# Optimization experiments

Hardware: AMD Instinct MI355X
Metric: run time of the kernel (lower is better)

The kernel has to match this reference:

```python
import jax, jax.numpy as jnp
import numpy as np

CPG = 2          # channels_per_group
WH, WW = 227, 227  # window_size
EPS = 1e-05


def setup_inputs() -> dict:
    key = jax.random.key(0)
    x = jax.random.normal(key, (8, 32, 512, 512), dtype=jnp.float32)
    weight = jnp.ones((1, 32, 1, 1), dtype=jnp.float32)
    bias = jnp.zeros((1, 32, 1, 1), dtype=jnp.float32)
    return {"x": x, "weight": weight, "bias": bias}


def _box_sum(ii, wh, ww):
    # ii: integral image (N,C,H,W); returns window sums of size (wh,ww)
    # over rows h+1..h+wh, cols w+1..w+ww -> (N,C,H-wh,W-ww)
    return (ii[:, :, wh:, ww:] - ii[:, :, :-wh, ww:]
            - ii[:, :, wh:, :-ww] + ii[:, :, :-wh, :-ww])


def reference(x, weight, bias):
    N, C, H, W = x.shape
    G = C // CPG
    # window_size (227,227) < (H,W)=(512,512): integral-image branch
    ii = jnp.cumsum(jnp.cumsum(x, axis=2), axis=3)
    ii_sq = jnp.cumsum(jnp.cumsum(x * x, axis=2), axis=3)
    h, w = H - WH, W - WW
    # per-channel box sums, then sum over channels_per_group -> (N,G,h,w)
    sums = _box_sum(ii, WH, WW).reshape(N, G, CPG, h, w).sum(axis=2)
    squares = _box_sum(ii_sq, WH, WW).reshape(N, G, CPG, h, w).sum(axis=2)
    n = WH * WW * CPG
    means = sums / n
    var = (squares - sums * sums / n) / n
    # replicate-pad stats back to (H,W): (left,right,top,bottom) like F.pad
    pt, pb = (H - h) // 2, H - h - (H - h) // 2
    pl, pr = (W - w) // 2, W - w - (W - w) // 2
    pad = ((0, 0), (0, 0), (pt, pb), (pl, pr))
    p_means = jnp.pad(means, pad, mode='edge')
    p_vars = jnp.pad(var, pad, mode='edge') + EPS
    # torch computes sums/squares under no_grad -> stats are constants
    p_means = jax.lax.stop_gradient(p_means)
    p_vars = jax.lax.stop_gradient(p_vars)
    xg = x.reshape(N, G, CPG, H, W)
    out = (xg - p_means[:, :, None]) / jnp.sqrt(p_vars)[:, :, None]
    out = out.reshape(N, C, H, W)
    return out * weight + bias
```

## Files before the change

### kernel.cpp

```cpp
#include <hip/hip_runtime.h>

namespace {
constexpr int Hn = 512, Wn = 512;
constexpr int WHn = 227, WWn = 227;
constexpr int OHn = Hn - WHn;
constexpr int OWn = Wn - WWn;
constexpr int PTn = 113, PLn = 113;
constexpr float EPSn = 1e-5f;
}

__global__ __launch_bounds__(512, 4) void lcn_fused(const float* __restrict__ x,
                                                    const float* __restrict__ weight,
                                                    const float* __restrict__ bias,
                                                    float* __restrict__ out) {
  const int B = blockIdx.x;
  const int X = B & 7;
  const int s = B >> 3;
  const int chunk = s & 3;
  const int g = X * 16 + (s >> 2);
  const int w = threadIdx.x;
  const int lane = w & 63;
  const int wid = w >> 6;

  const float* __restrict__ x0 = x + (size_t)(g * 2) * Hn * Wn;
  const float* __restrict__ x1 = x0 + (size_t)Hn * Wn;
  float* __restrict__ o0 = out + (size_t)(g * 2) * Hn * Wn;
  float* __restrict__ o1 = o0 + (size_t)Hn * Wn;
  const int cch = (g & 15) * 2;
  const float wt0 = weight[cch], wt1 = weight[cch + 1];
  const float bs0 = bias[cch], bs1 = bias[cch + 1];

  const int h0 = chunk == 0 ? 0 : chunk == 1 ? 48 : chunk == 2 ? 144 : 240;
  const int h1 = chunk == 0 ? 48 : chunk == 1 ? 144 : chunk == 2 ? 240 : 285;

  __shared__ __align__(16) float2 Ps[2][8][Wn + 1];
  __shared__ float2 wsum[8][8];
  __shared__ float2 bstat[4][132];

  const int q = w & 127;
  const int p = w >> 7;
  float4 sS = {0.f, 0.f, 0.f, 0.f}, sQ = {0.f, 0.f, 0.f, 0.f};
  {
    const float4* __restrict__ r0 =
        reinterpret_cast<const float4*>(x0 + (size_t)(h0 + 1) * Wn) + q;
    const float4* __restrict__ r1 =
        reinterpret_cast<const float4*>(x1 + (size_t)(h0 + 1) * Wn) + q;
    #pragma unroll 8
    for (int r = p; r < WHn; r += 4) {
      float4 a = r0[(size_t)r * (Wn / 4)];
      float4 b = r1[(size_t)r * (Wn / 4)];
      sS.x += a.x + b.x; sQ.x += a.x * a.x + b.x * b.x;
      sS.y += a.y + b.y; sQ.y += a.y * a.y + b.y * b.y;
      sS.z += a.z + b.z; sQ.z += a.z * a.z + b.z * b.z;
      sS.w += a.w + b.w; sQ.w += a.w * a.w + b.w * b.w;
    }
  }
  float accS, accQ;
  {
    float4* cc = reinterpret_cast<float4*>(&Ps[0][0][0]);
    cc[p * 256 + 2 * q]     = make_float4(sS.x, sQ.x, sS.y, sQ.y);
    cc[p * 256 + 2 * q + 1] = make_float4(sS.z, sQ.z, sS.w, sQ.w);
    __syncthreads();
    const float2* cf = reinterpret_cast<const float2*>(&Ps[0][0][0]);
    float2 t0 = cf[0 * Wn + w], t1 = cf[1 * Wn + w];
    float2 t2 = cf[2 * Wn + w], t3 = cf[3 * Wn + w];
    accS = (t0.x + t1.x) + (t2.x + t3.x);
    accQ = (t0.y + t1.y) + (t2.y + t3.y);
    __syncthreads();
  }

  const float inv_n = 1.0f / (float)(WHn * WWn * 2);
  const int wp = min(max(w - PLn, 0), OWn - 1);

  float pa0[8], pa1[8], ps0[8], ps1[8];
  auto prefetch = [&](int hb) {
    #pragma unroll
    for (int j = 0; j < 8; ++j) {
      int ra = min(hb + WHn + 1 + j, Hn - 1);
      int rs = hb + 1 + j;
      pa0[j] = x0[(size_t)ra * Wn + w];
      pa1[j] = x1[(size_t)ra * Wn + w];
      ps0[j] = x0[(size_t)rs * Wn + w];
      ps1[j] = x1[(size_t)rs * Wn + w];
    }
  };
  prefetch(h0);

  int buf = 0;
  for (int h = h0; h < h1; h += 8) {
    float2 v[8];
    v[0] = make_float2(accS, accQ);
    float s2 = accS, q2 = accQ;
    #pragma unroll
    for (int j = 0; j < 7; ++j) {
      s2 += (pa0[j] + pa1[j]) - (ps0[j] + ps1[j]);
      q2 += (pa0[j] * pa0[j] + pa1[j] * pa1[j])
          - (ps0[j] * ps0[j] + ps1[j] * ps1[j]);
      v[j + 1] = make_float2(s2, q2);
    }
    s2 += (pa0[7] + pa1[7]) - (ps0[7] + ps1[7]);
    q2 += (pa0[7] * pa0[7] + pa1[7] * pa1[7])
        - (ps0[7] * ps0[7] + ps1[7] * ps1[7]);
    accS = s2; accQ = q2;

    if (h + 8 < h1) prefetch(h + 8);
    float xa[8], xb[8];
    #pragma unroll
    for (int rr = 0; rr < 8; ++rr) {
      const size_t hh = (size_t)(h + PTn + rr) * Wn + w;
      xa[rr] = x0[hh];
      xb[rr] = x1[hh];
    }

    #pragma unroll
    for (int d = 1; d < 64; d <<= 1) {
      #pragma unroll
      for (int rr = 0; rr < 8; ++rr) {
        float sx = __shfl_up(v[rr].x, d, 64);
        float sy = __shfl_up(v[rr].y, d, 64);
        if (lane >= d) { v[rr].x += sx; v[rr].y += sy; }
      }
    }
    if (lane == 63) {
      #pragma unroll
      for (int rr = 0; rr < 8; ++rr) wsum[wid][rr] = v[rr];
    }
    __syncthreads();
    float2 off[8] = {{0.f,0.f},{0.f,0.f},{0.f,0.f},{0.f,0.f},
                     {0.f,0.f},{0.f,0.f},{0.f,0.f},{0.f,0.f}};
    #pragma unroll
    for (int i = 0; i < 7; ++i) {
      if (i < wid) {
        #pragma unroll
        for (int rr = 0; rr < 8; ++rr) {
          off[rr].x += wsum[i][rr].x; off[rr].y += wsum[i][rr].y;
        }
      }
    }
    #pragma unroll
    for (int rr = 0; rr < 8; ++rr)
      Ps[buf][rr][w + 1] = make_float2(v[rr].x + off[rr].x, v[rr].y + off[rr].y);
    __syncthreads();

    #pragma unroll
    for (int rr = 0; rr < 8; ++rr) {
      if (h + rr < h1) {
        float2 hi = Ps[buf][rr][wp + WWn + 1];
        float2 lo = Ps[buf][rr][wp + 1];
        float S = hi.x - lo.x;
        float Q = hi.y - lo.y;
        float mean = S * inv_n;
        float var = (Q - S * S * inv_n) * inv_n;
        float istd = rsqrtf(var + EPSn);
        if ((chunk == 0 && h + rr == 0) || (chunk == 3 && h + rr == 284))
          bstat[w & 3][w >> 2] = make_float2(mean, istd);
        const size_t oo = (size_t)(h + PTn + rr) * Wn + w;
        o0[oo] = (xa[rr] - mean) * istd * wt0 + bs0;
        o1[oo] = (xb[rr] - mean) * istd * wt1 + bs1;
      }
    }
    buf ^= 1;
  }

  if (chunk == 0 || chunk == 3) {
    __syncthreads();
    const int row0 = (chunk == 0) ? 0 : 398;
    const int nrows = (chunk == 0) ? PTn : Hn - 398;
    const int total = nrows * 256;
    const float4* __restrict__ xf0 = reinterpret_cast<const float4*>(x0);
    const float4* __restrict__ xf1 = reinterpret_cast<const float4*>(x1);
    float4* __restrict__ of0 = reinterpret_cast<float4*>(o0);
    float4* __restrict__ of1 = reinterpret_cast<float4*>(o1);
    for (int i = w; i < total; i += 512) {
      const int qq = i & 127;
      const int ch = (i >> 7) & 1;
      const int row = row0 + (i >> 8);
      const size_t idx = (size_t)row * (Wn / 4) + qq;
      const float4 xv = ch ? xf1[idx] : xf0[idx];
      const float wt = ch ? wt1 : wt0;
      const float bsv = ch ? bs1 : bs0;
      const float2 m0 = bstat[0][qq];
      const float2 m1 = bstat[1][qq];
      const float2 m2 = bstat[2][qq];
      const float2 m3 = bstat[3][qq];
      float4 ov;
      ov.x = (xv.x - m0.x) * m0.y * wt + bsv;
      ov.y = (xv.y - m1.x) * m1.y * wt + bsv;
      ov.z = (xv.z - m2.x) * m2.y * wt + bsv;
      ov.w = (xv.w - m3.x) * m3.y * wt + bsv;
      if (ch) of1[idx] = ov; else of0[idx] = ov;
    }
  }
}

extern "C" void kernel_launch(void* const* d_in, const int* in_sizes, int n_in,
                              void* d_out, int out_size, void* d_ws, size_t ws_size,
                              hipStream_t stream) {
  const float* x = (const float*)d_in[0];
  const float* weight = (const float*)d_in[1];
  const float* bias = (const float*)d_in[2];
  float* out = (float*)d_out;

  hipLaunchKernelGGL(lcn_fused, dim3(128 * 4), dim3(512), 0, stream,
                     x, weight, bias, out);
}
```

Measured before the change: 202.6 us.

## Precompute initial column-window sums in a separate segmented pre-pass kernel

Adds a pre-pass kernel that sums each group's rows in seven segments and combines those segment sums into the initial vertical window sums for all four row chunks. The main kernel loads these from workspace instead of each block reading 227 rows itself. This removes the overlapping reads between chunks (about 227 rows times 4 per group, versus roughly 467 rows shared) and rebalances the chunk boundaries. The cost is an extra kernel launch, a serial dependency between the two kernels, and a workspace round trip.

```diff
diff --git a/kernel.cpp b/kernel.cpp
--- a/kernel.cpp
+++ b/kernel.cpp
@@ -7,11 +7,82 @@
 constexpr int OWn = Wn - WWn;
 constexpr int PTn = 113, PLn = 113;
 constexpr float EPSn = 1e-5f;
+__device__ __constant__ int kH0[4] = {0, 46, 143, 240};
+__device__ __constant__ int kH1[4] = {46, 143, 240, 285};
+__device__ __constant__ int kSeg0[7] = {1, 47, 144, 228, 241, 274, 371};
+__device__ __constant__ int kSeg1[7] = {46, 143, 227, 240, 273, 370, 467};
+}
+
+__global__ __launch_bounds__(512, 4) void lcn_snap(const float* __restrict__ x,
+                                                   float2* __restrict__ snap) {
+  const int B = blockIdx.x;
+  const int g = B >> 2;
+  const int st = B & 3;
+  const int w = threadIdx.x;
+  const int q2 = w & 31;
+  const int p = w >> 5;
+
+  const float* __restrict__ x0 = x + (size_t)(g * 2) * Hn * Wn;
+  const float4* __restrict__ b0 =
+      reinterpret_cast<const float4*>(x0) + st * 32 + q2;
+  const float4* __restrict__ b1 = b0 + (size_t)Hn * (Wn / 4);
+
+  float4 sgS[7], sgQ[7];
+  #pragma unroll
+  for (int s = 0; s < 7; ++s) {
+    sgS[s] = make_float4(0.f, 0.f, 0.f, 0.f);
+    sgQ[s] = make_float4(0.f, 0.f, 0.f, 0.f);
+  }
+  #pragma unroll
+  for (int s = 0; s < 7; ++s) {
+    for (int r = kSeg0[s] + p; r <= kSeg1[s]; r += 16) {
+      float4 a = b0[(size_t)r * (Wn / 4)];
+      float4 b = b1[(size_t)r * (Wn / 4)];
+      sgS[s].x += a.x + b.x; sgQ[s].x += a.x * a.x + b.x * b.x;
+      sgS[s].y += a.y + b.y; sgQ[s].y += a.y * a.y + b.y * b.y;
+      sgS[s].z += a.z + b.z; sgQ[s].z += a.z * a.z + b.z * b.z;
+      sgS[s].w += a.w + b.w; sgQ[s].w += a.w * a.w + b.w * b.w;
+    }
+  }
+
+  __shared__ float4 tbuf[16][64];
+  float2 sg[7];
+  #pragma unroll
+  for (int s = 0; s < 7; ++s) {
+    __syncthreads();
+    tbuf[p][2 * q2]     = make_float4(sgS[s].x, sgQ[s].x, sgS[s].y, sgQ[s].y);
+    tbuf[p][2 * q2 + 1] = make_float4(sgS[s].z, sgQ[s].z, sgS[s].w, sgQ[s].w);
+    __syncthreads();
+    if (w < 128) {
+      const float2* cf = reinterpret_cast<const float2*>(&tbuf[0][0]);
+      float2 acc = {0.f, 0.f};
+      #pragma unroll
+      for (int pp = 0; pp < 16; ++pp) {
+        float2 t = cf[pp * 128 + w];
+        acc.x += t.x; acc.y += t.y;
+      }
+      sg[s] = acc;
+    }
+  }
+  if (w < 128) {
+    const float2 A = sg[0], Bs = sg[1], C = sg[2], D = sg[3],
+                 E = sg[4], F = sg[5], G = sg[6];
+    float2 w0 = {A.x + Bs.x + C.x, A.y + Bs.y + C.y};
+    float2 w1 = {Bs.x + C.x + D.x + E.x, Bs.y + C.y + D.y + E.y};
+    float2 w2 = {C.x + D.x + E.x + F.x, C.y + D.y + E.y + F.y};
+    float2 w3 = {E.x + F.x + G.x, E.y + F.y + G.y};
+    const size_t base = ((size_t)g * 4) * 512 + st * 128 + w;
+    snap[base]            = w0;
+    snap[base + 512]      = w1;
+    snap[base + 2 * 512]  = w2;
+    snap[base + 3 * 512]  = w3;
+  }
 }
 
 __global__ __launch_bounds__(512, 4) void lcn_fused(const float* __restrict__ x,
                                                     const float* __restrict__ weight,
                                                     const float* __restrict__ bias,
+                                                    const float2* __restrict__ snap,
                                                     float* __restrict__ out) {
   const int B = blockIdx.x;
   const int X = B & 7;
@@ -30,44 +101,15 @@
   const float wt0 = weight[cch], wt1 = weight[cch + 1];
   const float bs0 = bias[cch], bs1 = bias[cch + 1];
 
-  const int h0 = chunk == 0 ? 0 : chunk == 1 ? 48 : chunk == 2 ? 144 : 240;
-  const int h1 = chunk == 0 ? 48 : chunk == 1 ? 144 : chunk == 2 ? 240 : 285;
+  const int h0 = kH0[chunk];
+  const int h1 = kH1[chunk];
 
   __shared__ __align__(16) float2 Ps[2][8][Wn + 1];
   __shared__ float2 wsum[8][8];
   __shared__ float2 bstat[4][132];
 
-  const int q = w & 127;
-  const int p = w >> 7;
-  float4 sS = {0.f, 0.f, 0.f, 0.f}, sQ = {0.f, 0.f, 0.f, 0.f};
-  {
-    const float4* __restrict__ r0 =
-        reinterpret_cast<const float4*>(x0 + (size_t)(h0 + 1) * Wn) + q;
-    const float4* __restrict__ r1 =
-        reinterpret_cast<const float4*>(x1 + (size_t)(h0 + 1) * Wn) + q;
-    #pragma unroll 8
-    for (int r = p; r < WHn; r += 4) {
-      float4 a = r0[(size_t)r * (Wn / 4)];
-      float4 b = r1[(size_t)r * (Wn / 4)];
-      sS.x += a.x + b.x; sQ.x += a.x * a.x + b.x * b.x;
-      sS.y += a.y + b.y; sQ.y += a.y * a.y + b.y * b.y;
-      sS.z += a.z + b.z; sQ.z += a.z * a.z + b.z * b.z;
-      sS.w += a.w + b.w; sQ.w += a.w * a.w + b.w * b.w;
-    }
-  }
-  float accS, accQ;
-  {
-    float4* cc = reinterpret_cast<float4*>(&Ps[0][0][0]);
-    cc[p * 256 + 2 * q]     = make_float4(sS.x, sQ.x, sS.y, sQ.y);
-    cc[p * 256 + 2 * q + 1] = make_float4(sS.z, sQ.z, sS.w, sQ.w);
-    __syncthreads();
-    const float2* cf = reinterpret_cast<const float2*>(&Ps[0][0][0]);
-    float2 t0 = cf[0 * Wn + w], t1 = cf[1 * Wn + w];
-    float2 t2 = cf[2 * Wn + w], t3 = cf[3 * Wn + w];
-    accS = (t0.x + t1.x) + (t2.x + t3.x);
-    accQ = (t0.y + t1.y) + (t2.y + t3.y);
-    __syncthreads();
-  }
+  const float2 sv = snap[((size_t)(g * 4 + chunk)) * 512 + w];
+  float accS = sv.x, accQ = sv.y;
 
   const float inv_n = 1.0f / (float)(WHn * WWn * 2);
   const int wp = min(max(w - PLn, 0), OWn - 1);
@@ -200,7 +242,9 @@
   const float* weight = (const float*)d_in[1];
   const float* bias = (const float*)d_in[2];
   float* out = (float*)d_out;
-
-  hipLaunchKernelGGL(lcn_fused, dim3(128 * 4), dim3(512), 0, stream,
-                     x, weight, bias, out);
-}
+  float2* snap = (float2*)d_ws;
+
+  hipLaunchKernelGGL(lcn_snap, dim3(512), dim3(512), 0, stream, x, snap);
+  hipLaunchKernelGGL(lcn_fused, dim3(512), dim3(512), 0, stream,
+                     x, weight, bias, snap, out);
+}
```

Result: faster. 196.4 us (-3.0%).
